# Optimization experiments

Hardware: AMD Instinct MI355X
Metric: run time of the kernel (lower is better)

Reference implementation:

```python
import jax, jax.numpy as jnp
import numpy as np

K = 1  # top-k from init_kwargs


def setup_inputs() -> dict:
    key = jax.random.key(0)
    k0, k1, k2, k3, k4, k5 = jax.random.split(key, 6)
    B, L, Ed, NE = 8192, 1024, 1024, 8
    D = L + Ed  # input_dim = latent_dim + embed_dim
    s = 1.0 / np.sqrt(D)  # torch nn.Linear default init bound
    x = jax.random.normal(k0, (B, L), dtype=jnp.float32)
    y = jax.random.normal(k1, (B, Ed), dtype=jnp.float32)
    We = jax.random.uniform(k2, (NE, D, D), dtype=jnp.float32, minval=-s, maxval=s)  # expert weights [E, out, in]
    be = jax.random.uniform(k3, (NE, D), dtype=jnp.float32, minval=-s, maxval=s)
    gW = jax.random.uniform(k4, (NE, D), dtype=jnp.float32, minval=-s, maxval=s)  # gate weight [E, in]
    gb = jax.random.uniform(k5, (NE,), dtype=jnp.float32, minval=-s, maxval=s)
    return {"x": x, "y": y, "We": We, "be": be, "gW": gW, "gb": gb}


def reference(x, y, We, be, gW, gb):
    # inp: [B, D]
    inp = jnp.concatenate([x, y], axis=1)
    # gate logits: [B, E] (eval mode: no noise)
    gate_logits = inp @ gW.T + gb
    topk_val, topk_idx = jax.lax.top_k(gate_logits, K)  # [B, K]
    topk_gates = jax.nn.softmax(topk_val, axis=1)       # [B, K]
    # dense compute-all-experts (faithful to original): [B, E, D]
    all_out = jnp.einsum('bd,eod->beo', inp, We) + be[None, :, :]
    # gather top-k experts per token: [B, K, D]
    gathered = jnp.take_along_axis(all_out, topk_idx[:, :, None], axis=1)
    fused = jnp.sum(gathered * topk_gates[:, :, None], axis=1)  # [B, D]
    return fused
```

## Files before the change

### kernel.cpp

```cpp
#include <hip/hip_runtime.h>
#include <stdint.h>

#define B_TOK 8192
#define DIM   2048
#define NE    8
#define BM 128
#define BN 128
#define BK 64
#define CVT_BLOCKS 8192

typedef __bf16 bf16x8 __attribute__((ext_vector_type(8)));
typedef float  f32x4  __attribute__((ext_vector_type(4)));

__device__ __forceinline__ unsigned short f2b(float f) {
  unsigned u = __builtin_bit_cast(unsigned, f);
  u += 0x7fffu + ((u >> 16) & 1u);
  return (unsigned short)(u >> 16);
}
__device__ __forceinline__ uint2 pack4(float4 v) {
  uint2 r;
  r.x = (unsigned)f2b(v.x) | ((unsigned)f2b(v.y) << 16);
  r.y = (unsigned)f2b(v.z) | ((unsigned)f2b(v.w) << 16);
  return r;
}
__device__ __forceinline__ void gload16(const void* g, void* l) {
  __builtin_amdgcn_global_load_lds(
      (const __attribute__((address_space(1))) void*)g,
      (__attribute__((address_space(3))) void*)l, 16, 0, 0);
}

template <bool WINP>
__global__ __launch_bounds__(256) void gate_kernel(
    const float* __restrict__ x,
    const float* __restrict__ y,
    const float* __restrict__ gW,
    const float* __restrict__ gb,
    int* __restrict__ eid,
    unsigned short* __restrict__ inpB) {
  const int tid = threadIdx.x;
  const int ln = tid & 63;
  const int token = blockIdx.x * 4 + (tid >> 6);

  double acc[NE];
#pragma unroll
  for (int e = 0; e < NE; ++e) acc[e] = 0.0;

  const float* bases[2] = {x, y};
#pragma unroll
  for (int p = 0; p < 2; ++p) {
    const float* rowp = bases[p] + (size_t)token * 1024;
#pragma unroll
    for (int it = 0; it < 4; ++it) {
      const int d = it * 256 + ln * 4;
      float4 v = *(const float4*)(rowp + d);
      if (WINP)
        *(uint2*)(inpB + (size_t)token * DIM + p * 1024 + d) = pack4(v);
#pragma unroll
      for (int e = 0; e < NE; ++e) {
        float4 g = *(const float4*)(gW + e * DIM + p * 1024 + d);
        acc[e] += (double)v.x * (double)g.x + (double)v.y * (double)g.y +
                  (double)v.z * (double)g.z + (double)v.w * (double)g.w;
      }
    }
  }
#pragma unroll
  for (int e = 0; e < NE; ++e) {
#pragma unroll
    for (int off = 32; off >= 1; off >>= 1) acc[e] += __shfl_xor(acc[e], off, 64);
  }
  if (ln == 0) {
    int best = 0;
    double bv = acc[0] + (double)gb[0];
#pragma unroll
    for (int e = 1; e < NE; ++e) {
      double v = acc[e] + (double)gb[e];
      if (v > bv) { bv = v; best = e; }
    }
    eid[token] = best;
  }
}

template <bool CVT>
__global__ __launch_bounds__(256) void bucket_cvt(
    const int* __restrict__ eid,
    int* __restrict__ counts,
    int* __restrict__ perm,
    const float* __restrict__ We,
    unsigned short* __restrict__ WeB) {
  if (CVT && blockIdx.x >= NE) {
    const int cb = blockIdx.x - NE;
    const size_t base = (size_t)cb * 1024;
#pragma unroll
    for (int j = 0; j < 4; ++j) {
      size_t i4 = base + (size_t)(j * 256 + threadIdx.x);
      float4 v = *(const float4*)(We + i4 * 4);
      *(uint2*)(WeB + i4 * 4) = pack4(v);
    }
    return;
  }

  const int e = blockIdx.x;
  const int tid = threadIdx.x, ln = tid & 63, wv = tid >> 6;
  __shared__ int wsum[4];
  __shared__ int basev;
  if (tid == 0) basev = 0;
  __syncthreads();
  for (int t0 = 0; t0 < B_TOK; t0 += 256) {
    int t = t0 + tid;
    bool m = (eid[t] == e);
    unsigned long long mk = __ballot(m);
    int pre = __popcll(mk & ((1ull << ln) - 1ull));
    if (ln == 0) wsum[wv] = __popcll(mk);
    __syncthreads();
    int off = basev;
    for (int w = 0; w < wv; ++w) off += wsum[w];
    if (m) perm[e * B_TOK + off + pre] = t;
    __syncthreads();
    if (tid == 0) basev += wsum[0] + wsum[1] + wsum[2] + wsum[3];
    __syncthreads();
  }
  if (tid == 0) counts[e] = basev;
}

template <bool PRE>
__global__ __launch_bounds__(256) void moe_gemm(
    const float* __restrict__ x,
    const float* __restrict__ y,
    const float* __restrict__ We,
    const float* __restrict__ be,
    const unsigned short* __restrict__ inpB,
    const unsigned short* __restrict__ WeB,
    const int* __restrict__ counts,
    const int* __restrict__ perm,
    float* __restrict__ out) {
  __shared__ unsigned short As[BM * BK];
  __shared__ unsigned short Bs[BN * BK];
  __shared__ int tokLds[BM];

  const int e = blockIdx.z;
  const int cnt = counts[e];
  const int m0 = blockIdx.y * BM;
  if (m0 >= cnt) return;
  const int n0 = blockIdx.x * BN;

  const int tid = threadIdx.x;
  const int ln = tid & 63;
  const int wv = tid >> 6;
  const int wm = wv & 1, wn = wv >> 1;

  if (tid < BM) {
    int r = m0 + tid;
    tokLds[tid] = perm[e * B_TOK + (r < cnt ? r : cnt - 1)];
  }
  __syncthreads();

  const int cS = (ln & 7) ^ ((ln >> 3) & 7);
  int tokA[4], rowB[4];
#pragma unroll
  for (int j = 0; j < 4; ++j) {
    int row = (wv * 4 + j) * 8 + (ln >> 3);
    tokA[j] = tokLds[row];
    rowB[j] = row;
  }
  const unsigned short* wbbase = WeB + (size_t)e * DIM * DIM;
  const float* wfbase = We + (size_t)e * DIM * DIM;

  f32x4 acc[4][4];
#pragma unroll
  for (int i = 0; i < 4; ++i)
#pragma unroll
    for (int j = 0; j < 4; ++j) acc[i][j] = (f32x4){0.f, 0.f, 0.f, 0.f};

  for (int k0 = 0; k0 < DIM; k0 += BK) {
    __syncthreads();
    if constexpr (PRE) {
#pragma unroll
      for (int j = 0; j < 4; ++j) {
        gload16(inpB + (size_t)tokA[j] * DIM + k0 + cS * 8,
                &As[(wv * 4 + j) * 512]);
        gload16(wbbase + (size_t)(n0 + rowB[j]) * DIM + k0 + cS * 8,
                &Bs[(wv * 4 + j) * 512]);
      }
    } else {
      const float* ab = (k0 < 1024) ? x : y;
      const int kk = k0 & 1023;
#pragma unroll
      for (int i = 0; i < 8; ++i) {
        int li = i * 256 + tid;
        int row = li >> 4, k4 = li & 15;
        int chunk = k4 >> 1, half = k4 & 1;
        int slot = (chunk ^ (row & 7)) * 2 + half;
        int tok = tokLds[row];
        float4 va = *(const float4*)(ab + (size_t)tok * 1024 + kk + k4 * 4);
        *(uint2*)&As[row * BK + slot * 4] = pack4(va);
        float4 vb = *(const float4*)(wfbase + (size_t)(n0 + row) * DIM + k0 + k4 * 4);
        *(uint2*)&Bs[row * BK + slot * 4] = pack4(vb);
      }
    }
    __syncthreads();

#pragma unroll
    for (int ks = 0; ks < 2; ++ks) {
      bf16x8 av[4], bv[4];
#pragma unroll
      for (int i = 0; i < 4; ++i) {
        int rA = wm * 64 + i * 16 + (ln & 15);
        int c = ks * 4 + (ln >> 4);
        av[i] = *(const bf16x8*)&As[rA * BK + (c ^ (rA & 7)) * 8];
      }
#pragma unroll
      for (int j = 0; j < 4; ++j) {
        int rB = wn * 64 + j * 16 + (ln & 15);
        int c = ks * 4 + (ln >> 4);
        bv[j] = *(const bf16x8*)&Bs[rB * BK + (c ^ (rB & 7)) * 8];
      }
#pragma unroll
      for (int i = 0; i < 4; ++i)
#pragma unroll
        for (int j = 0; j < 4; ++j)
          acc[i][j] = __builtin_amdgcn_mfma_f32_16x16x32_bf16(av[i], bv[j], acc[i][j], 0, 0, 0);
    }
  }

  float bias[4]; int col[4];
#pragma unroll
  for (int j = 0; j < 4; ++j) {
    col[j] = n0 + wn * 64 + j * 16 + (ln & 15);
    bias[j] = be[e * DIM + col[j]];
  }
#pragma unroll
  for (int i = 0; i < 4; ++i) {
    int rbase = wm * 64 + i * 16 + ((ln >> 4) << 2);
#pragma unroll
    for (int r = 0; r < 4; ++r) {
      int rl = rbase + r;
      if (m0 + rl < cnt) {
        size_t t = (size_t)tokLds[rl];
#pragma unroll
        for (int j = 0; j < 4; ++j)
          out[t * DIM + col[j]] = acc[i][j][r] + bias[j];
      }
    }
  }
}

extern "C" void kernel_launch(void* const* d_in, const int* in_sizes, int n_in,
                              void* d_out, int out_size, void* d_ws, size_t ws_size,
                              hipStream_t stream) {
  const float* x  = (const float*)d_in[0];
  const float* y  = (const float*)d_in[1];
  const float* We = (const float*)d_in[2];
  const float* be = (const float*)d_in[3];
  const float* gW = (const float*)d_in[4];
  const float* gb = (const float*)d_in[5];
  float* out = (float*)d_out;

  char* ws = (char*)d_ws;
  int* counts = (int*)ws;
  int* eid    = (int*)(ws + 256);
  int* perm   = (int*)(ws + 33024);
  unsigned short* inpB = (unsigned short*)(ws + 295168);
  unsigned short* WeB  = (unsigned short*)(ws + 33849600);
  const size_t needed = 33849600ull + 67108864ull;

  if (ws_size >= needed) {
    gate_kernel<true><<<dim3(B_TOK / 4), 256, 0, stream>>>(x, y, gW, gb, eid, inpB);
    bucket_cvt<true><<<dim3(NE + CVT_BLOCKS), 256, 0, stream>>>(eid, counts, perm, We, WeB);
    moe_gemm<true><<<dim3(DIM / BN, B_TOK / BM, NE), 256, 0, stream>>>(
        x, y, We, be, inpB, WeB, counts, perm, out);
  } else {
    gate_kernel<false><<<dim3(B_TOK / 4), 256, 0, stream>>>(x, y, gW, gb, eid, nullptr);
    bucket_cvt<false><<<dim3(NE), 256, 0, stream>>>(eid, counts, perm, nullptr, nullptr);
    moe_gemm<false><<<dim3(DIM / BN, B_TOK / BM, NE), 256, 0, stream>>>(
        x, y, We, be, nullptr, nullptr, counts, perm, out);
  }
}
```

Baseline: 424.6 us.

## Add 4-stage async LDS pipeline with BK=32 to bf16 MoE GEMM

Replaces the single-buffered bf16 GEMM main loop with a 4-deep ring of LDS buffers, each holding a BK=32 slice, filled by global_load_lds. Prefetch runs three tiles ahead, synchronised with explicit vmcnt waits and raw s_barrier, so there is one barrier per step instead of two. MFMA priority is raised during compute, and launch bounds request two blocks per CU. The goal is to hide global load latency behind MFMA work, at the cost of 64KB of LDS per block, which may limit occupancy, and a fragile hand-counted wait scheme.

```diff
diff --git a/kernel.cpp b/kernel.cpp
--- a/kernel.cpp
+++ b/kernel.cpp
@@ -8,6 +8,9 @@
 #define BN 128
 #define BK 64
 #define CVT_BLOCKS 8192
+
+#define BK2 32
+#define NT2 (DIM / BK2)
 
 typedef __bf16 bf16x8 __attribute__((ext_vector_type(8)));
 typedef float  f32x4  __attribute__((ext_vector_type(4)));
@@ -122,19 +125,14 @@
   if (tid == 0) counts[e] = basev;
 }
 
-template <bool PRE>
-__global__ __launch_bounds__(256) void moe_gemm(
-    const float* __restrict__ x,
-    const float* __restrict__ y,
-    const float* __restrict__ We,
+__global__ __launch_bounds__(256, 2) void moe_gemm2(
     const float* __restrict__ be,
     const unsigned short* __restrict__ inpB,
     const unsigned short* __restrict__ WeB,
     const int* __restrict__ counts,
     const int* __restrict__ perm,
     float* __restrict__ out) {
-  __shared__ unsigned short As[BM * BK];
-  __shared__ unsigned short Bs[BN * BK];
+  __shared__ __align__(16) unsigned short AB[32768];
   __shared__ int tokLds[BM];
 
   const int e = blockIdx.z;
@@ -154,15 +152,121 @@
   }
   __syncthreads();
 
-  const int cS = (ln & 7) ^ ((ln >> 3) & 7);
-  int tokA[4], rowB[4];
+  const int srow0 = (wv * 2 + 0) * 16 + (ln >> 2);
+  const int srow1 = (wv * 2 + 1) * 16 + (ln >> 2);
+  const int g = (ln & 3) ^ ((ln >> 2) & 3);
+  const unsigned short* wbbase = WeB + (size_t)e * DIM * DIM;
+  const unsigned short* aSrc0 = inpB + (size_t)tokLds[srow0] * DIM + g * 8;
+  const unsigned short* aSrc1 = inpB + (size_t)tokLds[srow1] * DIM + g * 8;
+  const unsigned short* bSrc0 = wbbase + (size_t)(n0 + srow0) * DIM + g * 8;
+  const unsigned short* bSrc1 = wbbase + (size_t)(n0 + srow1) * DIM + g * 8;
+  const int dstA0 = (wv * 2 + 0) * 512;
+  const int dstA1 = (wv * 2 + 1) * 512;
+
+  const int slotR = (ln >> 4) ^ (ln & 3);
+  const int aOff = (wm * 64 + (ln & 15)) * 32 + slotR * 8;
+  const int bOff = (wn * 64 + (ln & 15)) * 32 + slotR * 8;
+
+  f32x4 acc[4][4];
+#pragma unroll
+  for (int i = 0; i < 4; ++i)
+#pragma unroll
+    for (int j = 0; j < 4; ++j) acc[i][j] = (f32x4){0.f, 0.f, 0.f, 0.f};
+
+  auto STAGE = [&](int kt) {
+    const int b = (kt & 3) * 4096;
+    const int ko = kt * BK2;
+    gload16(aSrc0 + ko, &AB[b + dstA0]);
+    gload16(aSrc1 + ko, &AB[b + dstA1]);
+    gload16(bSrc0 + ko, &AB[16384 + b + dstA0]);
+    gload16(bSrc1 + ko, &AB[16384 + b + dstA1]);
+  };
+  auto COMPUTE = [&](int kt) {
+    const int b = (kt & 3) * 4096;
+    bf16x8 av[4], bv[4];
+#pragma unroll
+    for (int i = 0; i < 4; ++i)
+      av[i] = *(const bf16x8*)&AB[b + aOff + i * 512];
+#pragma unroll
+    for (int j = 0; j < 4; ++j)
+      bv[j] = *(const bf16x8*)&AB[16384 + b + bOff + j * 512];
+    __builtin_amdgcn_s_setprio(1);
+#pragma unroll
+    for (int i = 0; i < 4; ++i)
+#pragma unroll
+      for (int j = 0; j < 4; ++j)
+        acc[i][j] = __builtin_amdgcn_mfma_f32_16x16x32_bf16(av[i], bv[j], acc[i][j], 0, 0, 0);
+    __builtin_amdgcn_s_setprio(0);
+  };
+
+  STAGE(0); STAGE(1); STAGE(2);
+  asm volatile("s_waitcnt vmcnt(8)" ::: "memory");
+  __builtin_amdgcn_s_barrier();
+
+  for (int t = 0; t < NT2; ++t) {
+    if (t + 3 < NT2) STAGE(t + 3);
+    COMPUTE(t);
+    if (t < NT2 - 3) {
+      asm volatile("s_waitcnt vmcnt(8)" ::: "memory");
+    } else if (t == NT2 - 3) {
+      asm volatile("s_waitcnt vmcnt(4)" ::: "memory");
+    } else if (t == NT2 - 2) {
+      asm volatile("s_waitcnt vmcnt(0)" ::: "memory");
+    }
+    if (t < NT2 - 1) __builtin_amdgcn_s_barrier();
+  }
+
+  float bias[4]; int col[4];
 #pragma unroll
   for (int j = 0; j < 4; ++j) {
-    int row = (wv * 4 + j) * 8 + (ln >> 3);
-    tokA[j] = tokLds[row];
-    rowB[j] = row;
-  }
-  const unsigned short* wbbase = WeB + (size_t)e * DIM * DIM;
+    col[j] = n0 + wn * 64 + j * 16 + (ln & 15);
+    bias[j] = be[e * DIM + col[j]];
+  }
+#pragma unroll
+  for (int i = 0; i < 4; ++i) {
+    int rbase = wm * 64 + i * 16 + ((ln >> 4) << 2);
+#pragma unroll
+    for (int r = 0; r < 4; ++r) {
+      int rl = rbase + r;
+      if (m0 + rl < cnt) {
+        size_t t = (size_t)tokLds[rl];
+#pragma unroll
+        for (int j = 0; j < 4; ++j)
+          out[t * DIM + col[j]] = acc[i][j][r] + bias[j];
+      }
+    }
+  }
+}
+
+__global__ __launch_bounds__(256) void moe_gemm_f32(
+    const float* __restrict__ x,
+    const float* __restrict__ y,
+    const float* __restrict__ We,
+    const float* __restrict__ be,
+    const int* __restrict__ counts,
+    const int* __restrict__ perm,
+    float* __restrict__ out) {
+  __shared__ unsigned short As[BM * BK];
+  __shared__ unsigned short Bs[BN * BK];
+  __shared__ int tokLds[BM];
+
+  const int e = blockIdx.z;
+  const int cnt = counts[e];
+  const int m0 = blockIdx.y * BM;
+  if (m0 >= cnt) return;
+  const int n0 = blockIdx.x * BN;
+
+  const int tid = threadIdx.x;
+  const int ln = tid & 63;
+  const int wv = tid >> 6;
+  const int wm = wv & 1, wn = wv >> 1;
+
+  if (tid < BM) {
+    int r = m0 + tid;
+    tokLds[tid] = perm[e * B_TOK + (r < cnt ? r : cnt - 1)];
+  }
+  __syncthreads();
+
   const float* wfbase = We + (size_t)e * DIM * DIM;
 
   f32x4 acc[4][4];
@@ -173,29 +277,19 @@
 
   for (int k0 = 0; k0 < DIM; k0 += BK) {
     __syncthreads();
-    if constexpr (PRE) {
-#pragma unroll
-      for (int j = 0; j < 4; ++j) {
-        gload16(inpB + (size_t)tokA[j] * DIM + k0 + cS * 8,
-                &As[(wv * 4 + j) * 512]);
-        gload16(wbbase + (size_t)(n0 + rowB[j]) * DIM + k0 + cS * 8,
-                &Bs[(wv * 4 + j) * 512]);
-      }
-    } else {
-      const float* ab = (k0 < 1024) ? x : y;
-      const int kk = k0 & 1023;
-#pragma unroll
-      for (int i = 0; i < 8; ++i) {
-        int li = i * 256 + tid;
-        int row = li >> 4, k4 = li & 15;
-        int chunk = k4 >> 1, half = k4 & 1;
-        int slot = (chunk ^ (row & 7)) * 2 + half;
-        int tok = tokLds[row];
-        float4 va = *(const float4*)(ab + (size_t)tok * 1024 + kk + k4 * 4);
-        *(uint2*)&As[row * BK + slot * 4] = pack4(va);
-        float4 vb = *(const float4*)(wfbase + (size_t)(n0 + row) * DIM + k0 + k4 * 4);
-        *(uint2*)&Bs[row * BK + slot * 4] = pack4(vb);
-      }
+    const float* ab = (k0 < 1024) ? x : y;
+    const int kk = k0 & 1023;
+#pragma unroll
+    for (int i = 0; i < 8; ++i) {
+      int li = i * 256 + tid;
+      int row = li >> 4, k4 = li & 15;
+      int chunk = k4 >> 1, half = k4 & 1;
+      int slot = (chunk ^ (row & 7)) * 2 + half;
+      int tok = tokLds[row];
+      float4 va = *(const float4*)(ab + (size_t)tok * 1024 + kk + k4 * 4);
+      *(uint2*)&As[row * BK + slot * 4] = pack4(va);
+      float4 vb = *(const float4*)(wfbase + (size_t)(n0 + row) * DIM + k0 + k4 * 4);
+      *(uint2*)&Bs[row * BK + slot * 4] = pack4(vb);
     }
     __syncthreads();
 
@@ -266,12 +360,12 @@
   if (ws_size >= needed) {
     gate_kernel<true><<<dim3(B_TOK / 4), 256, 0, stream>>>(x, y, gW, gb, eid, inpB);
     bucket_cvt<true><<<dim3(NE + CVT_BLOCKS), 256, 0, stream>>>(eid, counts, perm, We, WeB);
-    moe_gemm<true><<<dim3(DIM / BN, B_TOK / BM, NE), 256, 0, stream>>>(
-        x, y, We, be, inpB, WeB, counts, perm, out);
+    moe_gemm2<<<dim3(DIM / BN, B_TOK / BM, NE), 256, 0, stream>>>(
+        be, inpB, WeB, counts, perm, out);
   } else {
     gate_kernel<false><<<dim3(B_TOK / 4), 256, 0, stream>>>(x, y, gW, gb, eid, nullptr);
     bucket_cvt<false><<<dim3(NE), 256, 0, stream>>>(eid, counts, perm, nullptr, nullptr);
-    moe_gemm<false><<<dim3(DIM / BN, B_TOK / BM, NE), 256, 0, stream>>>(
-        x, y, We, be, nullptr, nullptr, counts, perm, out);
-  }
-}
+    moe_gemm_f32<<<dim3(DIM / BN, B_TOK / BM, NE), 256, 0, stream>>>(
+        x, y, We, be, counts, perm, out);
+  }
+}
```

Result: slower. 440.7 us (+3.8%).
